# Kernel optimization log

Hardware: AMD Instinct MI355X
Metric: run time of the kernel (lower is better)

## Reference

```python
import jax, jax.numpy as jnp
import numpy as np

IN_DIM, OUT_DIM = 256, 10
N_EXPERTS, N_MEM, STEPS, N_SUB, MAX_K = 12, 32, 6, 5, 5
EXPERT_DIMS = [2048, 2560, 3072, 3584, 4096, 2304, 2816, 3328, 3840, 4608, 3072, 4096]
MAX_E = 4608
N_ITEMS = 4096
SCALE = IN_DIM ** -0.5

def _gelu(x):
    return jax.nn.gelu(x, approximate=False)

_ACTS = [jax.nn.silu, _gelu, lambda x: x * jnp.tanh(jax.nn.softplus(x)), jax.nn.relu,
         jax.nn.selu, jnp.tanh, jax.nn.softplus, jax.nn.elu]
EXPERT_ACTS = [_ACTS[i % 8] for i in range(N_EXPERTS)]

def _ln(x, s, b, eps=1e-5):
    mu = jnp.mean(x, -1, keepdims=True)
    var = jnp.mean((x - mu) ** 2, -1, keepdims=True)
    return (x - mu) * jax.lax.rsqrt(var + eps) * s + b

def _cell(x, ln_s, ln_b, w1, b1, w2, b2):
    h = _gelu(_ln(x, ln_s, ln_b) @ w1.T + b1)
    return x + h @ w2.T + b2

def _ctx_attn(cur, bank, qw, kw, vw):
    q = cur @ qw.T
    k = bank @ kw.T
    v = bank @ vw.T
    attn = jax.nn.softmax(jnp.einsum('nd,ntd->nt', q, k) * SCALE, axis=-1)
    return jnp.einsum('nt,ntd->nd', attn, v)

def _renorm_sparse_topk(probs, active_k):
    tv, ti = jax.lax.top_k(probs, MAX_K)
    mask = (jnp.arange(MAX_K)[None, :] < active_k[:, None]).astype(probs.dtype)
    vals = tv * mask
    rows = jnp.arange(probs.shape[0])[:, None]
    sparse = jnp.zeros_like(probs).at[rows, ti].set(vals)
    return sparse / jnp.maximum(jnp.sum(sparse, -1, keepdims=True), 1e-6)

def _fwd(x, W, b,
         shared_up_w, shared_down_w, shared_ln_s, shared_ln_b, shared_scale,
         mem_keys, mem_vals, mem_q_w, mem_out_w, mem_wg_w, mem_wg_b, mem_wv_w, mem_wv_b,
         depth_q_w, depth_k_w, depth_v_w, depth_out_w,
         rc_ln_s, rc_ln_b, rc_w1, rc_b1, rc_w2, rc_b2,
         ssm_in_w, ssm_out_w, ssm_decay,
         sub_w, sub_b, gate_w, gate_b,
         budget_w, budget_b,
         exp_up, exp_down, exp_ln_s, exp_ln_b,
         halt_w, halt_b,
         aux_up_w, aux_down_w, aux_ln_s, aux_ln_b, aux_gate_w, aux_gate_b,
         rf_ln_s, rf_ln_b, rf_w1, rf_b1, rf_w2, rf_b2, reflect_out_w,
         coll_q_w, coll_k_w, coll_v_w, coll_out_w,
         revisit_w, revisit_b,
         vc_ln_s, vc_ln_b, vc_w1, vc_b1, vc_w2, vc_b2,
         ver_q_w, ver_k_w, ver_v_w, ver_out_w, ver_gate_w, ver_gate_b, correction_out_w,
         mix):
    n = x.shape[0]
    base = x @ W.T + b
    shared = _ln(jax.nn.silu(x @ shared_up_w.T) @ shared_down_w.T, shared_ln_s, shared_ln_b)
    aux = _ln(_gelu(x @ aux_up_w.T) @ aux_down_w.T, aux_ln_s, aux_ln_b)

    mem_vals_b = jnp.broadcast_to(mem_vals[None], (n, N_MEM, IN_DIM))
    current = x
    mem_logits = jnp.zeros_like(base)
    depth_logits = jnp.zeros_like(base)
    cum_halt = jnp.zeros((n, 1), x.dtype)
    bank = []
    for s in range(STEPS):
        q = current @ mem_q_w.T
        attn = jax.nn.softmax((q @ mem_keys.T) * SCALE, axis=-1)
        mem_read = jnp.einsum('ns,nsd->nd', attn, mem_vals_b)
        wg = jax.nn.sigmoid(jnp.concatenate([current, mem_read], -1) @ mem_wg_w.T + mem_wg_b)
        wv = current @ mem_wv_w.T + mem_wv_b
        mem_vals_b = mem_vals_b * (1.0 - wg[..., None]) + wg[..., None] * wv[:, None, :]
        if bank:
            depth_ctx = _ctx_attn(current, jnp.stack(bank, 1), depth_q_w, depth_k_w, depth_v_w)
        else:
            depth_ctx = jnp.zeros_like(current)
        current = _cell(current + mem_read + depth_ctx,
                        rc_ln_s[s], rc_ln_b[s], rc_w1[s], rc_b1[s], rc_w2[s], rc_b2[s])
        h = jnp.tanh(current @ ssm_in_w.T) * jax.nn.sigmoid(ssm_decay)
        current = current + h @ ssm_out_w.T
        bank.append(current)
        halt = jax.nn.sigmoid((current @ halt_w[s])[:, None] + halt_b[s])
        w_step = (1.0 - cum_halt) * halt
        mem_logits = mem_logits + w_step * (mem_read @ mem_out_w.T)
        depth_logits = depth_logits + w_step * (depth_ctx @ depth_out_w.T)
        cum_halt = jnp.minimum(cum_halt + halt, 1.0)

    sub_logits = jnp.einsum('nd,sed->nse', current, sub_w) + sub_b
    sub_probs = jax.nn.softmax(sub_logits, axis=-1)
    gate = jax.nn.softmax(current @ gate_w.T + gate_b, axis=-1)
    probs = jnp.einsum('ns,nse->ne', gate, sub_probs)
    active_k = jnp.argmax(current @ budget_w.T + budget_b, axis=-1) + 1
    sparse = _renorm_sparse_topk(probs, active_k)

    expert_out = jnp.zeros_like(base)
    for i in range(N_EXPERTS):
        h = EXPERT_ACTS[i](current @ exp_up[i].T)
        o = _ln(h @ exp_down[i].T, exp_ln_s[i], exp_ln_b[i])
        expert_out = expert_out + sparse[:, i:i + 1] * o

    r = current
    for i in range(3):
        r = _cell(r, rf_ln_s[i], rf_ln_b[i], rf_w1[i], rf_b1[i], rf_w2[i], rf_b2[i])
    reflect_logits = r @ reflect_out_w.T

    stack = jnp.stack(bank, 1)
    coll_ctx = _ctx_attn(current, stack, coll_q_w, coll_k_w, coll_v_w)
    coll_logits = coll_ctx @ coll_out_w.T
    revisit = jax.nn.sigmoid(jnp.concatenate([x, current, coll_ctx], -1) @ revisit_w.T + revisit_b)

    v = current
    for i in range(2):
        v = _cell(v, vc_ln_s[i], vc_ln_b[i], vc_w1[i], vc_b1[i], vc_w2[i], vc_b2[i])
    ver_ctx = _ctx_attn(v, stack, ver_q_w, ver_k_w, ver_v_w)
    vg = jax.nn.softmax(jnp.concatenate([v, ver_ctx], -1) @ ver_gate_w.T + ver_gate_b, axis=-1)
    ver_logits = ver_ctx @ ver_out_w.T
    corr_logits = v @ correction_out_w.T

    ag = jax.nn.softmax(x @ aux_gate_w.T + aux_gate_b, axis=-1)
    alpha, beta, gamma, delta, eps_, zeta = [jnp.tanh(mix[i]) for i in range(6)]
    logits = (base
              + shared_scale * (ag[:, :1] * shared + ag[:, 1:] * aux)
              + alpha * expert_out
              + beta * mem_logits + zeta * depth_logits
              + gamma * reflect_logits
              + delta * revisit * coll_logits
              + eps_ * (vg[:, :1] * ver_logits + vg[:, 1:] * corr_logits))
    return logits


def setup_inputs() -> dict:
    key = jax.random.key(0)
    ks = iter(jax.random.split(key, 128))
    def nrm(shape, std=0.02):
        return jax.random.normal(next(ks), shape, jnp.float32) * std
    d, o = IN_DIM, OUT_DIM
    inp = dict(
        x=jax.random.normal(next(ks), (N_ITEMS, d), jnp.float32),
        W=nrm((o, d), 0.05), b=jnp.zeros((o,), jnp.float32),
        shared_up_w=nrm((3072, d)), shared_down_w=nrm((o, 3072)),
        shared_ln_s=jnp.ones((o,)), shared_ln_b=jnp.zeros((o,)),
        shared_scale=jnp.float32(1.0),
        mem_keys=nrm((N_MEM, d)), mem_vals=nrm((N_MEM, d)),
        mem_q_w=nrm((d, d), 0.01), mem_out_w=nrm((o, d), 0.01),
        mem_wg_w=nrm((N_MEM, 2 * d), 0.01), mem_wg_b=jnp.zeros((N_MEM,)),
        mem_wv_w=nrm((d, d), 0.01), mem_wv_b=jnp.zeros((d,)),
        depth_q_w=nrm((d, d), 0.01), depth_k_w=nrm((d, d), 0.01),
        depth_v_w=nrm((d, d), 0.01), depth_out_w=nrm((o, d), 0.01),
        rc_ln_s=jnp.ones((STEPS, d)), rc_ln_b=jnp.zeros((STEPS, d)),
        rc_w1=nrm((STEPS, 896, d)), rc_b1=jnp.zeros((STEPS, 896)),
        rc_w2=nrm((STEPS, d, 896)), rc_b2=jnp.zeros((STEPS, d)),
        ssm_in_w=nrm((48, d)), ssm_out_w=nrm((d, 48)), ssm_decay=jnp.zeros((48,)),
        sub_w=nrm((N_SUB, N_EXPERTS, d)), sub_b=jnp.zeros((N_SUB, N_EXPERTS)),
        gate_w=nrm((N_SUB, d)), gate_b=jnp.zeros((N_SUB,)),
        budget_w=nrm((MAX_K, d), 0.01), budget_b=jnp.zeros((MAX_K,)),
        halt_w=nrm((STEPS, d), 0.01), halt_b=jnp.full((STEPS,), -2.0, jnp.float32),
        aux_up_w=nrm((4096, d)), aux_down_w=nrm((o, 4096)),
        aux_ln_s=jnp.ones((o,)), aux_ln_b=jnp.zeros((o,)),
        aux_gate_w=nrm((2, d), 0.01), aux_gate_b=jnp.zeros((2,)),
        rf_ln_s=jnp.ones((3, d)), rf_ln_b=jnp.zeros((3, d)),
        rf_w1=nrm((3, 1280, d)), rf_b1=jnp.zeros((3, 1280)),
        rf_w2=nrm((3, d, 1280)), rf_b2=jnp.zeros((3, d)),
        reflect_out_w=nrm((o, d), 0.01),
        coll_q_w=nrm((d, d), 0.01), coll_k_w=nrm((d, d), 0.01),
        coll_v_w=nrm((d, d), 0.01), coll_out_w=nrm((o, d), 0.01),
        revisit_w=nrm((1, 3 * d), 0.01), revisit_b=jnp.zeros((1,)),
        vc_ln_s=jnp.ones((2, d)), vc_ln_b=jnp.zeros((2, d)),
        vc_w1=nrm((2, 1536, d)), vc_b1=jnp.zeros((2, 1536)),
        vc_w2=nrm((2, d, 1536)), vc_b2=jnp.zeros((2, d)),
        ver_q_w=nrm((d, d), 0.01), ver_k_w=nrm((d, d), 0.01),
        ver_v_w=nrm((d, d), 0.01), ver_out_w=nrm((o, d), 0.01),
        ver_gate_w=nrm((2, 2 * d), 0.01), ver_gate_b=jnp.zeros((2,)),
        correction_out_w=nrm((o, d), 0.01),
        mix=jnp.full((6,), 0.5, jnp.float32),
    )
    up = jax.random.normal(next(ks), (N_EXPERTS, MAX_E, d), jnp.float32) * 0.02
    down = jax.random.normal(next(ks), (N_EXPERTS, o, MAX_E), jnp.float32) * 0.01
    col = jnp.arange(MAX_E)
    dims = jnp.array(EXPERT_DIMS)
    mask = (col[None, :] < dims[:, None]).astype(jnp.float32)
    inp['exp_up'] = up * mask[:, :, None]
    inp['exp_down'] = down * mask[:, None, :]
    inp['exp_ln_s'] = jnp.ones((N_EXPERTS, o))
    inp['exp_ln_b'] = jnp.zeros((N_EXPERTS, o))
    return inp


def reference(x, W, b,
              shared_up_w, shared_down_w, shared_ln_s, shared_ln_b, shared_scale,
              mem_keys, mem_vals, mem_q_w, mem_out_w, mem_wg_w, mem_wg_b, mem_wv_w, mem_wv_b,
              depth_q_w, depth_k_w, depth_v_w, depth_out_w,
              rc_ln_s, rc_ln_b, rc_w1, rc_b1, rc_w2, rc_b2,
              ssm_in_w, ssm_out_w, ssm_decay,
              sub_w, sub_b, gate_w, gate_b,
              budget_w, budget_b,
              exp_up, exp_down, exp_ln_s, exp_ln_b,
              halt_w, halt_b,
              aux_up_w, aux_down_w, aux_ln_s, aux_ln_b, aux_gate_w, aux_gate_b,
              rf_ln_s, rf_ln_b, rf_w1, rf_b1, rf_w2, rf_b2, reflect_out_w,
              coll_q_w, coll_k_w, coll_v_w, coll_out_w,
              revisit_w, revisit_b,
              vc_ln_s, vc_ln_b, vc_w1, vc_b1, vc_w2, vc_b2,
              ver_q_w, ver_k_w, ver_v_w, ver_out_w, ver_gate_w, ver_gate_b, correction_out_w,
              mix):
    return _fwd(x, W, b,
                shared_up_w, shared_down_w, shared_ln_s, shared_ln_b, shared_scale,
                mem_keys, mem_vals, mem_q_w, mem_out_w, mem_wg_w, mem_wg_b, mem_wv_w, mem_wv_b,
                depth_q_w, depth_k_w, depth_v_w, depth_out_w,
                rc_ln_s, rc_ln_b, rc_w1, rc_b1, rc_w2, rc_b2,
                ssm_in_w, ssm_out_w, ssm_decay,
                sub_w, sub_b, gate_w, gate_b,
                budget_w, budget_b,
                exp_up, exp_down, exp_ln_s, exp_ln_b,
                halt_w, halt_b,
                aux_up_w, aux_down_w, aux_ln_s, aux_ln_b, aux_gate_w, aux_gate_b,
                rf_ln_s, rf_ln_b, rf_w1, rf_b1, rf_w2, rf_b2, reflect_out_w,
                coll_q_w, coll_k_w, coll_v_w, coll_out_w,
                revisit_w, revisit_b,
                vc_ln_s, vc_ln_b, vc_w1, vc_b1, vc_w2, vc_b2,
                ver_q_w, ver_k_w, ver_v_w, ver_out_w, ver_gate_w, ver_gate_b, correction_out_w,
                mix)
```

## Files before the change

kernel.cpp:

```cpp
#include <hip/hip_runtime.h>


constexpr int NI      = 4096;
constexpr int DIM     = 256;
constexpr int ODIM    = 10;
constexpr int NMEM_   = 32;
constexpr int NSTEPS_ = 6;
constexpr int NEXPERT_= 12;
constexpr int MAXE    = 4608;
constexpr int TOTCOL  = 46592;
constexpr int NGRP    = 182;
#define SCL 0.0625f

__constant__ int GCNT[14]   = {8,10,12,14,16,9,11,13,15,18,12,16,12,16};
__constant__ int GSTART[14] = {0,8,18,30,44,60,69,80,93,108,126,138,154,166};
__constant__ int CCNT[14]   = {32,40,48,56,64,36,44,52,60,72,48,64,48,64};
__constant__ int ZCOL[14]   = {0,2048,4608,7680,11264,15360,17664,20480,
                               23808,27648,32256,35328,39424,42496};

typedef __attribute__((ext_vector_type(8))) short short8v;
typedef __attribute__((ext_vector_type(4))) float float4v;
typedef __attribute__((ext_vector_type(4))) unsigned short ushort4v;


__device__ __forceinline__ float wred_sum(float v){
  #pragma unroll
  for (int m = 32; m > 0; m >>= 1) v += __shfl_xor(v, m, 64);
  return v;
}
__device__ __forceinline__ float wred_max(float v){
  #pragma unroll
  for (int m = 32; m > 0; m >>= 1) v = fmaxf(v, __shfl_xor(v, m, 64));
  return v;
}
__device__ __forceinline__ float sigm(float x){ return 1.f/(1.f + __expf(-x)); }
__device__ __forceinline__ float tanh_f(float x){
  float e = __expf(2.f*fabsf(x));
  float r = 1.f - 2.f/(e + 1.f);
  return copysignf(r, x);
}
__device__ __forceinline__ float erf_f(float x){
  float ax = fabsf(x);
  float t = 1.f/fmaf(0.3275911f, ax, 1.f);
  float p = t*(0.254829592f + t*(-0.284496736f + t*(1.421413741f +
            t*(-1.453152027f + t*1.061405429f))));
  float r = 1.f - p*__expf(-ax*ax);
  return copysignf(r, x);
}
__device__ __forceinline__ float geluf(float x){
  return 0.5f*x*(1.f + erf_f(x*0.70710678118654752f));
}
__device__ __forceinline__ float softplusf(float x){
  return fmaxf(x, 0.f) + __logf(1.f + __expf(-fabsf(x)));
}
__device__ __forceinline__ float act_apply(int a, float x){
  switch(a){
    case 0: return x*sigm(x);
    case 1: return geluf(x);
    case 2: return x*tanh_f(softplusf(x));
    case 3: return fmaxf(x, 0.f);
    case 4: { const float l=1.0507009873554805f, al=1.6732632423543772f;
              return x > 0.f ? l*x : l*al*(__expf(x)-1.f); }
    case 5: return tanh_f(x);
    case 6: return softplusf(x);
    default: return x > 0.f ? x : __expf(x)-1.f;
  }
}
__device__ __forceinline__ unsigned short f2b(float f){
  unsigned u = __float_as_uint(f);
  u = u + 0x7FFFu + ((u >> 16) & 1u);
  return (unsigned short)(u >> 16);
}
__device__ __forceinline__ float b2f(unsigned short u){
  return __uint_as_float((unsigned)u << 16);
}
__device__ __forceinline__ float dot256f(const float* __restrict__ a,
                                         const float* __restrict__ w, float s){
  for (int k = 0; k < DIM; k += 4){
    float4 av = *(const float4*)&a[k];
    float4 wv = *(const float4*)&w[k];
    s = fmaf(av.x,wv.x, fmaf(av.y,wv.y, fmaf(av.z,wv.z, fmaf(av.w,wv.w, s))));
  }
  return s;
}
__device__ __forceinline__ void ln10(const float* p, const float* s, const float* b, float* o){
  float mu = 0.f;
  #pragma unroll
  for (int i=0;i<ODIM;i++) mu += p[i];
  mu *= 0.1f;
  float var = 0.f;
  #pragma unroll
  for (int i=0;i<ODIM;i++){ float d = p[i]-mu; var += d*d; }
  var *= 0.1f;
  float rs = 1.f/sqrtf(var + 1e-5f);
  #pragma unroll
  for (int i=0;i<ODIM;i++) o[i] = (p[i]-mu)*rs*s[i] + b[i];
}

__global__ __launch_bounds__(256)
void cvt_k(const float* __restrict__ in, unsigned short* __restrict__ out, int n)
{
  int idx = (blockIdx.x*256 + threadIdx.x)*4;
  if (idx + 3 < n){
    float4 v = *(const float4*)&in[idx];
    ushort4v t; t[0]=f2b(v.x); t[1]=f2b(v.y); t[2]=f2b(v.z); t[3]=f2b(v.w);
    *(ushort4v*)&out[idx] = t;
  }
}

__global__ __launch_bounds__(512)
void cvtup_k(const float* __restrict__ exp_up, const float* __restrict__ shared_up,
             const float* __restrict__ aux_up, short* __restrict__ upb)
{
  int chunk = blockIdx.x;
  int z = 0, crem = chunk;
  while (crem >= CCNT[z]){ crem -= CCNT[z]; z++; }
  const float* src;
  if (z < 12)       src = exp_up + (size_t)z*MAXE*DIM;
  else if (z == 12) src = shared_up;
  else              src = aux_up;
  int colbase = crem*64;
  short* dst = upb + (size_t)chunk*16384;
  int t = threadIdx.x;
  int c = t >> 3, kb = (t & 7)*32;
  const float* srow = src + (size_t)(colbase + c)*DIM + kb;
  #pragma unroll
  for (int j = 0; j < 4; j++){
    float4 f0 = *(const float4*)&srow[j*8];
    float4 f1 = *(const float4*)&srow[j*8+4];
    short8v s;
    s[0]=(short)f2b(f0.x); s[1]=(short)f2b(f0.y); s[2]=(short)f2b(f0.z); s[3]=(short)f2b(f0.w);
    s[4]=(short)f2b(f1.x); s[5]=(short)f2b(f1.y); s[6]=(short)f2b(f1.z); s[7]=(short)f2b(f1.w);
    int kq = (t & 7)*4 + j;
    *(short8v*)&dst[((size_t)kq*64 + c)*8] = s;
  }
}

template<int EPI>
__global__ __launch_bounds__(256)
void gemm_k(const float* __restrict__ A, const float* __restrict__ W,
            const float* __restrict__ bias, const float* __restrict__ R,
            float* __restrict__ C, float* __restrict__ C2, int N, int K)
{
  __shared__ float As[32][68];
  __shared__ float Ws[32][68];
  const int bm = blockIdx.y*64, bn = blockIdx.x*64;
  const int tid = threadIdx.x;
  const int tx = tid & 15, ty = tid >> 4;
  const int lrow = tid >> 2, lkq = (tid & 3) * 8;
  float acc[4][4] = {};
  for (int k0 = 0; k0 < K; k0 += 32){
    #pragma unroll
    for (int h = 0; h < 2; ++h){
      int kk = lkq + h*4;
      float4 va = *(const float4*)&A[(size_t)(bm+lrow)*K + k0 + kk];
      float4 vw = *(const float4*)&W[(size_t)(bn+lrow)*K + k0 + kk];
      As[kk+0][lrow]=va.x; As[kk+1][lrow]=va.y; As[kk+2][lrow]=va.z; As[kk+3][lrow]=va.w;
      Ws[kk+0][lrow]=vw.x; Ws[kk+1][lrow]=vw.y; Ws[kk+2][lrow]=vw.z; Ws[kk+3][lrow]=vw.w;
    }
    __syncthreads();
    #pragma unroll
    for (int kk = 0; kk < 32; ++kk){
      float4 a4 = *(const float4*)&As[kk][ty*4];
      float4 b4 = *(const float4*)&Ws[kk][tx*4];
      float av[4] = {a4.x,a4.y,a4.z,a4.w};
      float bv[4] = {b4.x,b4.y,b4.z,b4.w};
      #pragma unroll
      for (int i=0;i<4;i++)
        #pragma unroll
        for (int j=0;j<4;j++) acc[i][j] = fmaf(av[i], bv[j], acc[i][j]);
    }
    __syncthreads();
  }
  #pragma unroll
  for (int i=0;i<4;i++){
    int r = bm + ty*4 + i;
    #pragma unroll
    for (int j=0;j<4;j++){
      int c = bn + tx*4 + j;
      float v = acc[i][j];
      if constexpr (EPI==0){ C[(size_t)r*N + c] = v; }
      else if constexpr (EPI==1){ C[(size_t)r*N + c] = v + bias[c]; }
      else if constexpr (EPI==2){ C[(size_t)r*N + c] = geluf(v + bias[c]); }
      else if constexpr (EPI==3){ C[(size_t)r*N + c] = v + bias[c] + R[(size_t)r*N + c]; }
      else if constexpr (EPI==6){
        if (c < 256) C[(size_t)r*256 + c] = v + bias[c];
        else C2[(size_t)r*256 + (c-256)] = v;
      }
    }
  }
}

template<int EPI>
__global__ __launch_bounds__(256)
void bgemm_k(const short* __restrict__ A, const short* __restrict__ B,
             const float* __restrict__ bias, const float* __restrict__ R,
             float* __restrict__ Cf, unsigned short* __restrict__ Cb,
             int N, int K)
{
  __shared__ short As[128][40];
  __shared__ short Bsm[64][40];
  const int bm = blockIdx.y*128, bn = blockIdx.x*64;
  const int tid = threadIdx.x;
  const int wave = tid >> 6, lane = tid & 63;
  const int l15 = lane & 15, lg = lane >> 4;
  const int ar = tid >> 1, ah = tid & 1;
  float4v acc[2][4] = {};
  for (int k0 = 0; k0 < K; k0 += 32){
    __syncthreads();
    { const short* src = A + (size_t)(bm+ar)*K + k0 + ah*16;
      short8v v0 = *(const short8v*)src;
      short8v v1 = *(const short8v*)(src+8);
      *(short8v*)&As[ar][ah*16]   = v0;
      *(short8v*)&As[ar][ah*16+8] = v1; }
    if (tid < 128){
      const short* src = B + (size_t)(bn+ar)*K + k0 + ah*16;
      short8v v0 = *(const short8v*)src;
      short8v v1 = *(const short8v*)(src+8);
      *(short8v*)&Bsm[ar][ah*16]   = v0;
      *(short8v*)&Bsm[ar][ah*16+8] = v1; }
    __syncthreads();
    short8v bfr[4];
    #pragma unroll
    for (int nt = 0; nt < 4; nt++)
      bfr[nt] = *(const short8v*)&Bsm[nt*16 + l15][lg*8];
    #pragma unroll
    for (int mt = 0; mt < 2; mt++){
      short8v a = *(const short8v*)&As[wave*32 + mt*16 + l15][lg*8];
      #pragma unroll
      for (int nt = 0; nt < 4; nt++)
        acc[mt][nt] = __builtin_amdgcn_mfma_f32_16x16x32_bf16(a, bfr[nt], acc[mt][nt], 0, 0, 0);
    }
  }
  #pragma unroll
  for (int mt = 0; mt < 2; mt++)
    #pragma unroll
    for (int nt = 0; nt < 4; nt++)
      #pragma unroll
      for (int reg = 0; reg < 4; reg++){
        int row = bm + wave*32 + mt*16 + lg*4 + reg;
        int col = bn + nt*16 + l15;
        float v = acc[mt][nt][reg];
        if constexpr (EPI==0){
          v = geluf(v + bias[col]);
          Cb[(size_t)row*N + col] = f2b(v);
        } else {
          v = v + bias[col] + R[(size_t)row*N + col];
          Cf[(size_t)row*N + col] = v;
        }
      }
}

__global__ __launch_bounds__(512)
void moe4_k(const unsigned short* __restrict__ curb, const unsigned short* __restrict__ xb,
            const short* __restrict__ upb,
            const float* __restrict__ exp_down, const float* __restrict__ shared_down,
            const float* __restrict__ aux_down,
            unsigned short* __restrict__ part)
{
  __shared__ short Bs[16384];
  __shared__ float Ds[64][12];
  const int g = blockIdx.y;
  int gy = g, z = 0;
  while (gy >= GCNT[z]){ gy -= GCNT[z]; z++; }
  const int localcol = gy*256;
  int act, dstride; const float* down;
  if (z < 12){ act = z & 7; down = exp_down + (size_t)z*ODIM*MAXE; dstride = MAXE; }
  else if (z == 12){ act = 0; down = shared_down; dstride = 3072; }
  else { act = 1; down = aux_down; dstride = 4096; }
  const unsigned short* X = (z < 12) ? curb : xb;
  const int bm = blockIdx.x*128;
  const int tid = threadIdx.x, wave = tid >> 6, lane = tid & 63;
  const int l15 = lane & 15, lg = lane >> 4;

  short8v afrag[8];
  { const unsigned short* xr = X + (size_t)(bm + wave*16 + l15)*DIM;
    #pragma unroll
    for (int ks = 0; ks < 8; ks++)
      afrag[ks] = *(const short8v*)&xr[ks*32 + lg*8];
  }
  float racc[4][10];
  #pragma unroll
  for (int r = 0; r < 4; r++)
    #pragma unroll
    for (int o = 0; o < 10; o++) racc[r][o] = 0.f;

  const int gchunk0 = (ZCOL[z] + localcol) >> 6;
  const int dso = tid >> 6, dse = tid & 63;

  auto ld = [&](int ch, short8v* p, float& d0, float& d1){
    const short* chunk = upb + ((size_t)(gchunk0 + ch))*16384;
    #pragma unroll
    for (int i = 0; i < 4; i++)
      p[i] = *(const short8v*)&chunk[(size_t)(tid + 512*i)*8];
    int cb = localcol + ch*64;
    d0 = down[(size_t)dso*dstride + cb + dse];
    d1 = (tid < 128) ? down[(size_t)(dso+8)*dstride + cb + dse] : 0.f;
  };

  short8v preA[4], preB[4];
  float dA0, dA1, dB0, dB1;
  ld(0, preA, dA0, dA1);
  #pragma unroll
  for (int ch = 0; ch < 4; ch++){
    const short8v* P = (ch & 1) ? preB : preA;
    float d0 = (ch & 1) ? dB0 : dA0;
    float d1 = (ch & 1) ? dB1 : dA1;
    #pragma unroll
    for (int i = 0; i < 4; i++){
      int u = tid + 512*i;
      int c = u & 63, kq = u >> 6;
      int byteoff = ((c << 9) + (kq << 4)) ^ ((c & 7) << 4);
      *(short8v*)((char*)Bs + byteoff) = P[i];
    }
    Ds[dse][dso] = d0;
    if (tid < 128) Ds[dse][dso + 8] = d1;
    __syncthreads();
    if (ch < 3){
      if (ch & 1) ld(ch + 1, preA, dA0, dA1);
      else        ld(ch + 1, preB, dB0, dB1);
    }
    float4v acc[4] = {};
    #pragma unroll
    for (int ks = 0; ks < 8; ks++)
      #pragma unroll
      for (int nt = 0; nt < 4; nt++){
        int c = nt*16 + l15, kq = ks*4 + lg;
        int byteoff = ((c << 9) + (kq << 4)) ^ ((c & 7) << 4);
        short8v b = *(const short8v*)((const char*)Bs + byteoff);
        acc[nt] = __builtin_amdgcn_mfma_f32_16x16x32_bf16(afrag[ks], b, acc[nt], 0, 0, 0);
      }
    #pragma unroll
    for (int nt = 0; nt < 4; nt++){
      const float* dp = &Ds[nt*16 + l15][0];
      float4 dv0 = *(const float4*)dp;
      float4 dv1 = *(const float4*)(dp + 4);
      float  d8 = dp[8], d9 = dp[9];
      float dv[10] = {dv0.x,dv0.y,dv0.z,dv0.w,dv1.x,dv1.y,dv1.z,dv1.w,d8,d9};
      float hv[4];
      #pragma unroll
      for (int reg = 0; reg < 4; reg++) hv[reg] = act_apply(act, acc[nt][reg]);
      #pragma unroll
      for (int o = 0; o < 10; o++)
        #pragma unroll
        for (int reg = 0; reg < 4; reg++)
          racc[reg][o] = fmaf(hv[reg], dv[o], racc[reg][o]);
    }
    __syncthreads();
  }
  #pragma unroll
  for (int reg = 0; reg < 4; reg++)
    #pragma unroll
    for (int o = 0; o < 10; o++){
      float v = racc[reg][o];
      v += __shfl_xor(v, 1, 64); v += __shfl_xor(v, 2, 64);
      v += __shfl_xor(v, 4, 64); v += __shfl_xor(v, 8, 64);
      racc[reg][o] = v;
    }
  if (l15 == 0){
    #pragma unroll
    for (int reg = 0; reg < 4; reg++){
      int row = bm + wave*16 + lg*4 + reg;
      #pragma unroll
      for (int o = 0; o < 10; o++)
        part[((size_t)g*NI + row)*ODIM + o] = f2b(racc[reg][o]);
    }
  }
}

__global__ __launch_bounds__(256)
void red_k(const unsigned short* __restrict__ part, float* __restrict__ expert_pre,
           float* __restrict__ shared_pre, float* __restrict__ aux_pre)
{
  int idx = blockIdx.x*256 + threadIdx.x;
  if (idx >= 14*NI*ODIM) return;
  int z = idx / (NI*ODIM), rem = idx - z*NI*ODIM;
  float s = 0.f;
  int g0 = GSTART[z], gn = GCNT[z];
  for (int g2 = 0; g2 < gn; g2++)
    s += b2f(part[(size_t)(g0 + g2)*NI*ODIM + rem]);
  if (z < 12) expert_pre[(size_t)z*NI*ODIM + rem] = s;
  else if (z == 12) shared_pre[rem] = s;
  else aux_pre[rem] = s;
}

__global__ void atb_k(const float* __restrict__ A, const float* __restrict__ B,
                      float* __restrict__ C, int M, int I, int J)
{
  int idx = blockIdx.x*256 + threadIdx.x;
  if (idx >= I*J) return;
  int i = idx / J, j = idx - i*J;
  float s = 0.f;
  for (int m = 0; m < M; m++) s = fmaf(A[(size_t)m*I+i], B[(size_t)m*J+j], s);
  C[idx] = s;
}
__global__ void ab_k(const float* __restrict__ A, const float* __restrict__ B,
                     float* __restrict__ C, int M, int K, int N)
{
  int idx = blockIdx.x*256 + threadIdx.x;
  if (idx >= M*N) return;
  int i = idx / N, j = idx - i*N;
  float s = 0.f;
  for (int k = 0; k < K; k++) s = fmaf(A[(size_t)i*K+k], B[(size_t)k*N+j], s);
  C[idx] = s;
}

__global__ __launch_bounds__(256)
void ln3_k(const float* __restrict__ a, const float* __restrict__ b,
           const float* __restrict__ c, const float* __restrict__ lns,
           const float* __restrict__ lnb, float* __restrict__ xout,
           float* __restrict__ lnout, unsigned short* __restrict__ lnout_b)
{
  int item = blockIdx.x*4 + (threadIdx.x >> 6);
  int lane = threadIdx.x & 63;
  float4 v = ((const float4*)(a + (size_t)item*DIM))[lane];
  if (b){ float4 t = ((const float4*)(b + (size_t)item*DIM))[lane]; v.x+=t.x; v.y+=t.y; v.z+=t.z; v.w+=t.w; }
  if (c){ float4 t = ((const float4*)(c + (size_t)item*DIM))[lane]; v.x+=t.x; v.y+=t.y; v.z+=t.z; v.w+=t.w; }
  if (xout) ((float4*)(xout + (size_t)item*DIM))[lane] = v;
  float mu = wred_sum(v.x+v.y+v.z+v.w) * (1.f/DIM);
  float dx=v.x-mu, dy=v.y-mu, dz=v.z-mu, dw=v.w-mu;
  float var = wred_sum(dx*dx+dy*dy+dz*dz+dw*dw) * (1.f/DIM);
  float rs = 1.f/sqrtf(var + 1e-5f);
  float4 s4 = ((const float4*)lns)[lane];
  float4 b4 = ((const float4*)lnb)[lane];
  float4 o4 = make_float4(dx*rs*s4.x + b4.x, dy*rs*s4.y + b4.y,
                          dz*rs*s4.z + b4.z, dw*rs*s4.w + b4.w);
  if (lnout) ((float4*)(lnout + (size_t)item*DIM))[lane] = o4;
  if (lnout_b){
    ushort4v t; t[0]=f2b(o4.x); t[1]=f2b(o4.y); t[2]=f2b(o4.z); t[3]=f2b(o4.w);
    *(ushort4v*)(lnout_b + (size_t)item*DIM + lane*4) = t;
  }
}

__global__ __launch_bounds__(256)
void memrw_k(const float* __restrict__ cur, const float* __restrict__ MK,
             const float* __restrict__ mem_vals, const float* __restrict__ wv_hist,
             const float* __restrict__ mem_wg_w, const float* __restrict__ mem_wg_b,
             float* __restrict__ a_state, float* __restrict__ c_state,
             float* __restrict__ mem_read, int step)
{
  __shared__ float smem[4][DIM];
  int wi = threadIdx.x >> 6;
  int item = blockIdx.x*4 + wi;
  int lane = threadIdx.x & 63;
  float v = -1e30f;
  if (lane < NMEM_)
    v = dot256f(cur + (size_t)item*DIM, MK + (size_t)lane*DIM, 0.f) * SCL;
  float m = wred_max(v);
  float e = (lane < NMEM_) ? __expf(v - m) : 0.f;
  float inv = 1.f / wred_sum(e);
  float attn = e * inv;
  float aval = 0.f;
  if (lane < NMEM_) aval = (step == 0) ? 1.f : a_state[(size_t)item*NMEM_ + lane];
  float wslot = attn * aval;
  float beta[NSTEPS_];
  #pragma unroll
  for (int t = 0; t < NSTEPS_; t++){
    beta[t] = 0.f;
    if (t < step){
      float cc = (lane < NMEM_) ? c_state[((size_t)item*NMEM_ + lane)*NSTEPS_ + t] : 0.f;
      beta[t] = wred_sum(attn * cc);
    }
  }
  float ax=0.f, ay=0.f, az=0.f, aw=0.f;
  #pragma unroll
  for (int s2 = 0; s2 < NMEM_; s2++){
    float ws = __shfl(wslot, s2, 64);
    float4 mv = ((const float4*)(mem_vals + (size_t)s2*DIM))[lane];
    ax = fmaf(ws, mv.x, ax); ay = fmaf(ws, mv.y, ay);
    az = fmaf(ws, mv.z, az); aw = fmaf(ws, mv.w, aw);
  }
  #pragma unroll
  for (int t = 0; t < NSTEPS_; t++){
    if (t < step){
      float4 h4 = ((const float4*)(wv_hist + ((size_t)t*NI + item)*DIM))[lane];
      ax = fmaf(beta[t], h4.x, ax); ay = fmaf(beta[t], h4.y, ay);
      az = fmaf(beta[t], h4.z, az); aw = fmaf(beta[t], h4.w, aw);
    }
  }
  float4 mr = make_float4(ax,ay,az,aw);
  ((float4*)(mem_read + (size_t)item*DIM))[lane] = mr;
  ((float4*)&smem[wi][0])[lane] = mr;
  __syncthreads();
  if (lane < NMEM_){
    const float* wr = mem_wg_w + (size_t)lane*2*DIM;
    float s = dot256f(cur + (size_t)item*DIM, wr, 0.f);
    s = dot256f(&smem[wi][0], wr + DIM, s);
    s += mem_wg_b[lane];
    float gte = sigm(s);
    int idx = item*NMEM_ + lane;
    float om = 1.f - gte;
    float a = (step == 0) ? 1.f : a_state[idx];
    a_state[idx] = a * om;
    float* c = c_state + (size_t)idx*NSTEPS_;
// ... 317 lines not shown
  const float* rc_ln_b       = (const float*)d_in[21];
  const float* rc_w1         = (const float*)d_in[22];
  const float* rc_b1         = (const float*)d_in[23];
  const float* rc_w2         = (const float*)d_in[24];
  const float* rc_b2         = (const float*)d_in[25];
  const float* ssm_in_w      = (const float*)d_in[26];
  const float* ssm_out_w     = (const float*)d_in[27];
  const float* ssm_decay     = (const float*)d_in[28];
  const float* sub_w         = (const float*)d_in[29];
  const float* sub_b         = (const float*)d_in[30];
  const float* gate_w        = (const float*)d_in[31];
  const float* gate_b        = (const float*)d_in[32];
  const float* budget_w      = (const float*)d_in[33];
  const float* budget_b      = (const float*)d_in[34];
  const float* halt_w        = (const float*)d_in[35];
  const float* halt_b        = (const float*)d_in[36];
  const float* aux_up_w      = (const float*)d_in[37];
  const float* aux_down_w    = (const float*)d_in[38];
  const float* aux_ln_s      = (const float*)d_in[39];
  const float* aux_ln_b      = (const float*)d_in[40];
  const float* aux_gate_w    = (const float*)d_in[41];
  const float* aux_gate_b    = (const float*)d_in[42];
  const float* rf_ln_s       = (const float*)d_in[43];
  const float* rf_ln_b       = (const float*)d_in[44];
  const float* rf_w1         = (const float*)d_in[45];
  const float* rf_b1         = (const float*)d_in[46];
  const float* rf_w2         = (const float*)d_in[47];
  const float* rf_b2         = (const float*)d_in[48];
  const float* reflect_out_w = (const float*)d_in[49];
  const float* coll_q_w      = (const float*)d_in[50];
  const float* coll_k_w      = (const float*)d_in[51];
  const float* coll_v_w      = (const float*)d_in[52];
  const float* coll_out_w    = (const float*)d_in[53];
  const float* revisit_w     = (const float*)d_in[54];
  const float* revisit_b     = (const float*)d_in[55];
  const float* vc_ln_s       = (const float*)d_in[56];
  const float* vc_ln_b       = (const float*)d_in[57];
  const float* vc_w1         = (const float*)d_in[58];
  const float* vc_b1         = (const float*)d_in[59];
  const float* vc_w2         = (const float*)d_in[60];
  const float* vc_b2         = (const float*)d_in[61];
  const float* ver_q_w       = (const float*)d_in[62];
  const float* ver_k_w       = (const float*)d_in[63];
  const float* ver_v_w       = (const float*)d_in[64];
  const float* ver_out_w     = (const float*)d_in[65];
  const float* ver_gate_w    = (const float*)d_in[66];
  const float* ver_gate_b    = (const float*)d_in[67];
  const float* correction_out_w = (const float*)d_in[68];
  const float* mix           = (const float*)d_in[69];
  const float* exp_up        = (const float*)d_in[70];
  const float* exp_down      = (const float*)d_in[71];
  const float* exp_ln_s      = (const float*)d_in[72];
  const float* exp_ln_b      = (const float*)d_in[73];
  float* out = (float*)d_out;

  float* w = (float*)d_ws;
  size_t off = 0;
  auto WS = [&](size_t nf){ float* p = w + off; off += nf; return p; };
  float* bank      = WS((size_t)NSTEPS_*NI*DIM);
  float* rbuf      = WS((size_t)NI*DIM);
  float* vbuf      = WS((size_t)NI*DIM);
  float* coll_ctx  = WS((size_t)NI*DIM);
  float* ver_ctx   = WS((size_t)NI*DIM);
  float* q2        = WS((size_t)NI*DIM);
  float* wsumb     = WS((size_t)NI*DIM);
  float* sparse    = WS((size_t)NI*NEXPERT_);
  float* base10    = WS((size_t)NI*ODIM);
  float* reflect10 = WS((size_t)NI*ODIM);
  float* coll10    = WS((size_t)NI*ODIM);
  float* ver10     = WS((size_t)NI*ODIM);
  float* corr10    = WS((size_t)NI*ODIM);
  float* PcT       = WS((size_t)DIM*DIM);
  float* PvT       = WS((size_t)DIM*DIM);
  float* MK        = WS((size_t)NMEM_*DIM);
  float* Wvq       = WS((size_t)512*DIM);
  float* expert_pre= WS((size_t)NEXPERT_*NI*ODIM);
  float* shared_pre= WS((size_t)NI*ODIM);
  float* aux_pre   = WS((size_t)NI*ODIM);
  unsigned short* cur_b = (unsigned short*)WS((size_t)NI*DIM/2);
  unsigned short* x_b   = (unsigned short*)WS((size_t)NI*DIM/2);
  float* zbase     = w + off;
  float* mem_logits   = WS((size_t)NI*ODIM);
  float* depth_logits = WS((size_t)NI*ODIM);
  float* cum_halt     = WS((size_t)NI);
  size_t zbytes = (size_t)((w + off) - zbase) * sizeof(float);
  hipMemsetAsync((void*)zbase, 0, zbytes, stream);

  float* U = w + off;
  float* wv_hist   = U;
  float* hbig      = U + (size_t)NSTEPS_*NI*DIM;
  float* cur_in    = hbig + (size_t)NI*896;
  float* t_ln      = cur_in + (size_t)NI*DIM;
  float* mem_read  = t_ln + (size_t)NI*DIM;
  float* depth_ctx = mem_read + (size_t)NI*DIM;
  float* a_state   = depth_ctx + (size_t)NI*DIM;
  float* c_state   = a_state + (size_t)NI*NMEM_;
  unsigned short* upb    = (unsigned short*)U;
  unsigned short* hb     = (unsigned short*)U;
  float* ovl = U + 5963776;
  unsigned short* t_ln_b = (unsigned short*)ovl;          ovl += 524288;
  unsigned short* rfw1b  = (unsigned short*)ovl;          ovl += 491520;
  unsigned short* rfw2b  = (unsigned short*)ovl;          ovl += 491520;
  unsigned short* vcw1b  = (unsigned short*)ovl;          ovl += 393216;
  unsigned short* vcw2b  = (unsigned short*)ovl;          ovl += 393216;
  unsigned short* part   = (unsigned short*)ovl;

  hipMemcpyAsync(Wvq, mem_wv_w, (size_t)DIM*DIM*sizeof(float),
                 hipMemcpyDeviceToDevice, stream);
  atb_k<<<(DIM*DIM+255)/256, 256, 0, stream>>>(depth_k_w, depth_q_w, Wvq + (size_t)DIM*DIM, DIM, DIM, DIM);
  atb_k<<<(DIM*DIM+255)/256, 256, 0, stream>>>(coll_k_w,  coll_q_w,  PcT, DIM, DIM, DIM);
  atb_k<<<(DIM*DIM+255)/256, 256, 0, stream>>>(ver_k_w,   ver_q_w,   PvT, DIM, DIM, DIM);
  ab_k <<<(NMEM_*DIM+255)/256, 256, 0, stream>>>(mem_keys, mem_q_w, MK, NMEM_, DIM, DIM);

  const float* cur = x;
  for (int s = 0; s < NSTEPS_; s++){
    memrw_k<<<NI/4, 256, 0, stream>>>(cur, MK, mem_vals, wv_hist,
                                      mem_wg_w, mem_wg_b, a_state, c_state,
                                      mem_read, s);
    gemm_k<6><<<dim3(8, NI/64), 256, 0, stream>>>(
        cur, Wvq, mem_wv_b, nullptr, wv_hist + (size_t)s*NI*DIM, q2, 512, DIM);
    if (s > 0){
      bankattn_k<<<NI/4, 256, 0, stream>>>(q2, bank, wsumb, s);
      gemm_k<0><<<dim3(4, NI/64), 256, 0, stream>>>(
          wsumb, depth_v_w, nullptr, nullptr, depth_ctx, nullptr, DIM, DIM);
    }
    ln3_k<<<NI/4, 256, 0, stream>>>(cur, mem_read, (s > 0 ? depth_ctx : nullptr),
                                    rc_ln_s + (size_t)s*DIM, rc_ln_b + (size_t)s*DIM,
                                    cur_in, t_ln, nullptr);
    gemm_k<2><<<dim3(14, NI/64), 256, 0, stream>>>(
        t_ln, rc_w1 + (size_t)s*896*DIM, rc_b1 + (size_t)s*896, nullptr,
        hbig, nullptr, 896, DIM);
    gemm_k<3><<<dim3(4, NI/64), 256, 0, stream>>>(
        hbig, rc_w2 + (size_t)s*DIM*896, rc_b2 + (size_t)s*DIM, cur_in,
        cur_in, nullptr, DIM, 896);
    float* newcur = bank + (size_t)s*NI*DIM;
    ssmhalt_k<<<NI/4, 256, 0, stream>>>(cur_in, mem_read, depth_ctx,
                                        ssm_in_w, ssm_out_w, ssm_decay,
                                        halt_w, halt_b, mem_out_w, depth_out_w,
                                        newcur, mem_logits, depth_logits, cum_halt, s);
    cur = newcur;
  }

  router2_k<<<NI/4, 256, 0, stream>>>(cur, sub_w, sub_b, gate_w, gate_b,
                                      budget_w, budget_b, sparse);

  launch_cvt(cur, cur_b, (size_t)NI*DIM, stream);
  launch_cvt(x,   x_b,   (size_t)NI*DIM, stream);
  cvtup_k<<<TOTCOL/64, 512, 0, stream>>>(exp_up, shared_up_w, aux_up_w, (short*)upb);
  launch_cvt(rf_w1, rfw1b, (size_t)3*1280*DIM, stream);
  launch_cvt(rf_w2, rfw2b, (size_t)3*DIM*1280, stream);
  launch_cvt(vc_w1, vcw1b, (size_t)2*1536*DIM, stream);
  launch_cvt(vc_w2, vcw2b, (size_t)2*DIM*1536, stream);

  moe4_k<<<dim3(NI/128, NGRP), 512, 0, stream>>>(
      cur_b, x_b, (const short*)upb, exp_down, shared_down_w, aux_down_w, part);
  red_k<<<(14*NI*ODIM + 255)/256, 256, 0, stream>>>(part, expert_pre, shared_pre, aux_pre);

  const float* rsrc = cur;
  for (int i = 0; i < 3; i++){
    ln3_k<<<NI/4, 256, 0, stream>>>(rsrc, nullptr, nullptr,
                                    rf_ln_s + (size_t)i*DIM, rf_ln_b + (size_t)i*DIM,
                                    nullptr, nullptr, t_ln_b);
    bgemm_k<0><<<dim3(1280/64, NI/128), 256, 0, stream>>>(
        (const short*)t_ln_b, (const short*)(rfw1b + (size_t)i*1280*DIM),
        rf_b1 + (size_t)i*1280, nullptr, nullptr, hb, 1280, DIM);
    bgemm_k<1><<<dim3(DIM/64, NI/128), 256, 0, stream>>>(
        (const short*)hb, (const short*)(rfw2b + (size_t)i*DIM*1280),
        rf_b2 + (size_t)i*DIM, rsrc, rbuf, nullptr, DIM, 1280);
    rsrc = rbuf;
  }

  const float* vsrc = cur;
  for (int i = 0; i < 2; i++){
    ln3_k<<<NI/4, 256, 0, stream>>>(vsrc, nullptr, nullptr,
                                    vc_ln_s + (size_t)i*DIM, vc_ln_b + (size_t)i*DIM,
                                    nullptr, nullptr, t_ln_b);
    bgemm_k<0><<<dim3(1536/64, NI/128), 256, 0, stream>>>(
        (const short*)t_ln_b, (const short*)(vcw1b + (size_t)i*1536*DIM),
        vc_b1 + (size_t)i*1536, nullptr, nullptr, hb, 1536, DIM);
    bgemm_k<1><<<dim3(DIM/64, NI/128), 256, 0, stream>>>(
        (const short*)hb, (const short*)(vcw2b + (size_t)i*DIM*1536),
        vc_b2 + (size_t)i*DIM, vsrc, vbuf, nullptr, DIM, 1536);
    vsrc = vbuf;
  }

  gemm_k<0><<<dim3(4, NI/64), 256, 0, stream>>>(
      cur, PcT, nullptr, nullptr, q2, nullptr, DIM, DIM);
  bankattn_k<<<NI/4, 256, 0, stream>>>(q2, bank, wsumb, NSTEPS_);
  gemm_k<0><<<dim3(4, NI/64), 256, 0, stream>>>(
      wsumb, coll_v_w, nullptr, nullptr, coll_ctx, nullptr, DIM, DIM);

  gemm_k<0><<<dim3(4, NI/64), 256, 0, stream>>>(
      vbuf, PvT, nullptr, nullptr, q2, nullptr, DIM, DIM);
  bankattn_k<<<NI/4, 256, 0, stream>>>(q2, bank, wsumb, NSTEPS_);
  gemm_k<0><<<dim3(4, NI/64), 256, 0, stream>>>(
      wsumb, ver_v_w, nullptr, nullptr, ver_ctx, nullptr, DIM, DIM);

  heads_k<<<(NI*50 + 255)/256, 256, 0, stream>>>(
      rbuf, coll_ctx, ver_ctx, vbuf, x,
      reflect_out_w, coll_out_w, ver_out_w, correction_out_w, Wm, bvec,
      reflect10, coll10, ver10, corr10, base10);

  final_k<<<(NI+255)/256, 256, 0, stream>>>(
      x, cur, vbuf, coll_ctx, ver_ctx,
      base10, shared_pre, aux_pre, expert_pre, sparse,
      mem_logits, depth_logits, reflect10, coll10, ver10, corr10,
      shared_ln_s, shared_ln_b, aux_ln_s, aux_ln_b, exp_ln_s, exp_ln_b,
      aux_gate_w, aux_gate_b, ver_gate_w, ver_gate_b, revisit_w, revisit_b,
      shared_scale, mix, out);
}
```

Baseline: 3.264 ms.

## Split MoE kernel into per-activation templated launches and simplify prefetch buffers

Replaces the single MoE launch, whose activation was chosen at runtime per block, with eight launches of a kernel templated on the activation type. Each launch covers the experts that share that activation, so the runtime activation branch and the group-search loop go away. The double-buffered register prefetch is also reduced to a single set of registers loaded after the barrier, which lowers register pressure. The costs are eight kernel launches in place of one, smaller grids per launch that may underfill the GPU, and possibly less overlap between loads and compute.

```diff
diff --git a/kernel.cpp b/kernel.cpp
--- a/kernel.cpp
+++ b/kernel.cpp
@@ -9,7 +9,6 @@
 constexpr int NEXPERT_= 12;
 constexpr int MAXE    = 4608;
 constexpr int TOTCOL  = 46592;
-constexpr int NGRP    = 182;
 #define SCL 0.0625f
 
 __constant__ int GCNT[14]   = {8,10,12,14,16,9,11,13,15,18,12,16,12,16};
@@ -251,23 +250,29 @@
       }
 }
 
+template<int ACT>
 __global__ __launch_bounds__(512)
-void moe4_k(const unsigned short* __restrict__ curb, const unsigned short* __restrict__ xb,
+void moe5_k(const unsigned short* __restrict__ curb, const unsigned short* __restrict__ xb,
             const short* __restrict__ upb,
             const float* __restrict__ exp_down, const float* __restrict__ shared_down,
             const float* __restrict__ aux_down,
-            unsigned short* __restrict__ part)
+            unsigned short* __restrict__ part,
+            int z0, int z1, int z2)
 {
   __shared__ short Bs[16384];
   __shared__ float Ds[64][12];
-  const int g = blockIdx.y;
-  int gy = g, z = 0;
-  while (gy >= GCNT[z]){ gy -= GCNT[z]; z++; }
+  int gy = blockIdx.y;
+  int z = z0;
+  if (z1 >= 0 && gy >= GCNT[z]){
+    gy -= GCNT[z]; z = z1;
+    if (z2 >= 0 && gy >= GCNT[z]){ gy -= GCNT[z]; z = z2; }
+  }
+  const int g = GSTART[z] + gy;
   const int localcol = gy*256;
-  int act, dstride; const float* down;
-  if (z < 12){ act = z & 7; down = exp_down + (size_t)z*ODIM*MAXE; dstride = MAXE; }
-  else if (z == 12){ act = 0; down = shared_down; dstride = 3072; }
-  else { act = 1; down = aux_down; dstride = 4096; }
+  int dstride; const float* down;
+  if (z < 12){ down = exp_down + (size_t)z*ODIM*MAXE; dstride = MAXE; }
+  else if (z == 12){ down = shared_down; dstride = 3072; }
+  else { down = aux_down; dstride = 4096; }
   const unsigned short* X = (z < 12) ? curb : xb;
   const int bm = blockIdx.x*128;
   const int tid = threadIdx.x, wave = tid >> 6, lane = tid & 63;
@@ -288,38 +293,31 @@
   const int gchunk0 = (ZCOL[z] + localcol) >> 6;
   const int dso = tid >> 6, dse = tid & 63;
 
-  auto ld = [&](int ch, short8v* p, float& d0, float& d1){
+  short8v p0, p1, p2, p3;
+  float e0, e1;
+  auto ldchunk = [&](int ch){
     const short* chunk = upb + ((size_t)(gchunk0 + ch))*16384;
-    #pragma unroll
-    for (int i = 0; i < 4; i++)
-      p[i] = *(const short8v*)&chunk[(size_t)(tid + 512*i)*8];
+    p0 = *(const short8v*)&chunk[(size_t)(tid       )*8];
+    p1 = *(const short8v*)&chunk[(size_t)(tid +  512)*8];
+    p2 = *(const short8v*)&chunk[(size_t)(tid + 1024)*8];
+    p3 = *(const short8v*)&chunk[(size_t)(tid + 1536)*8];
     int cb = localcol + ch*64;
-    d0 = down[(size_t)dso*dstride + cb + dse];
-    d1 = (tid < 128) ? down[(size_t)(dso+8)*dstride + cb + dse] : 0.f;
+    e0 = down[(size_t)dso*dstride + cb + dse];
+    e1 = (tid < 128) ? down[(size_t)(dso+8)*dstride + cb + dse] : 0.f;
   };
-
-  short8v preA[4], preB[4];
-  float dA0, dA1, dB0, dB1;
-  ld(0, preA, dA0, dA1);
-  #pragma unroll
-  for (int ch = 0; ch < 4; ch++){
-    const short8v* P = (ch & 1) ? preB : preA;
-    float d0 = (ch & 1) ? dB0 : dA0;
-    float d1 = (ch & 1) ? dB1 : dA1;
-    #pragma unroll
-    for (int i = 0; i < 4; i++){
-      int u = tid + 512*i;
-      int c = u & 63, kq = u >> 6;
-      int byteoff = ((c << 9) + (kq << 4)) ^ ((c & 7) << 4);
-      *(short8v*)((char*)Bs + byteoff) = P[i];
-    }
-    Ds[dse][dso] = d0;
-    if (tid < 128) Ds[dse][dso + 8] = d1;
+  auto stu = [&](int u, short8v v){
+    int c = u & 63, kq = u >> 6;
+    int byteoff = ((c << 9) + (kq << 4)) ^ ((c & 7) << 4);
+    *(short8v*)((char*)Bs + byteoff) = v;
+  };
+
+  ldchunk(0);
+  for (int ch = 0; ch < 4; ++ch){
+    stu(tid, p0); stu(tid + 512, p1); stu(tid + 1024, p2); stu(tid + 1536, p3);
+    Ds[dse][dso] = e0;
+    if (tid < 128) Ds[dse][dso + 8] = e1;
     __syncthreads();
-    if (ch < 3){
-      if (ch & 1) ld(ch + 1, preA, dA0, dA1);
-      else        ld(ch + 1, preB, dB0, dB1);
-    }
+    if (ch < 3) ldchunk(ch + 1);
     float4v acc[4] = {};
     #pragma unroll
     for (int ks = 0; ks < 8; ks++)
@@ -339,7 +337,7 @@
       float dv[10] = {dv0.x,dv0.y,dv0.z,dv0.w,dv1.x,dv1.y,dv1.z,dv1.w,d8,d9};
       float hv[4];
       #pragma unroll
-      for (int reg = 0; reg < 4; reg++) hv[reg] = act_apply(act, acc[nt][reg]);
+      for (int reg = 0; reg < 4; reg++) hv[reg] = act_apply(ACT, acc[nt][reg]);
       #pragma unroll
       for (int o = 0; o < 10; o++)
         #pragma unroll
@@ -963,8 +961,21 @@
   launch_cvt(vc_w1, vcw1b, (size_t)2*1536*DIM, stream);
   launch_cvt(vc_w2, vcw2b, (size_t)2*DIM*1536, stream);
 
-  moe4_k<<<dim3(NI/128, NGRP), 512, 0, stream>>>(
-      cur_b, x_b, (const short*)upb, exp_down, shared_down_w, aux_down_w, part);
+  {
+    #define MOE_LAUNCH(ACT, NG, Z0, Z1, Z2)                                   \
+      moe5_k<ACT><<<dim3(NI/128, NG), 512, 0, stream>>>(                      \
+          cur_b, x_b, (const short*)upb, exp_down, shared_down_w, aux_down_w, \
+          part, Z0, Z1, Z2)
+    MOE_LAUNCH(1, 44, 1, 9, 13);
+    MOE_LAUNCH(0, 35, 0, 8, 12);
+    MOE_LAUNCH(3, 30, 3, 11, -1);
+    MOE_LAUNCH(2, 24, 2, 10, -1);
+    MOE_LAUNCH(4, 16, 4, -1, -1);
+    MOE_LAUNCH(7, 13, 7, -1, -1);
+    MOE_LAUNCH(6, 11, 6, -1, -1);
+    MOE_LAUNCH(5,  9, 5, -1, -1);
+    #undef MOE_LAUNCH
+  }
   red_k<<<(14*NI*ODIM + 255)/256, 256, 0, stream>>>(part, expert_pre, shared_pre, aux_pre);
 
   const float* rsrc = cur;
```

New measurement: 2.822 ms. -13.6%, faster.
